# Kernel tuning notes

Hardware: AMD Instinct MI355X
Metric: run time of the kernel (lower is better)

Reference implementation:

```python
import jax, jax.numpy as jnp
from jax import lax
import numpy as np

STRIDES = (2, 2)
PADDING = 'SAME'
EPS = 1e-05


def setup_inputs() -> dict:
    key = jax.random.key(0)
    k1, k2, k3 = jax.random.split(key, 3)
    x = jax.random.normal(k1, (16, 64, 64, 256), dtype=jnp.float32)
    # flax default conv kernel init ~ lecun_normal; plain normal scaled is fine for a math reference
    kernel = jax.random.normal(k2, (4, 4, 256, 128), dtype=jnp.float32) * 0.05
    bias = jax.random.normal(k3, (128,), dtype=jnp.float32) * 0.01
    alpha = jnp.ones((1,), dtype=jnp.float32)
    return {'x': x, 'kernel': kernel, 'bias': bias, 'alpha': alpha}


def reference(x, kernel, bias, alpha):
    # x: [B, H, W, Cin] NHWC; kernel: [kh, kw, Cin, Cout]
    out_features = kernel.shape[-1]

    # main transposed conv: dot-product map  [B, H*2, W*2, Cout]
    dot = lax.conv_transpose(x, kernel, STRIDES, PADDING, transpose_kernel=False)

    # patch squared-sum map: conv_transpose of x**2 with an all-ones kernel
    # of shape kernel_size + (Cin, 1); broadcast over Cout (same math as jnp.repeat)
    ones_k = jnp.ones(kernel.shape[:-1] + (1,), dtype=kernel.dtype)
    patch_sq = lax.conv_transpose(x * x, ones_k, STRIDES, PADDING, transpose_kernel=False)  # [B, H', W', 1]

    # per-filter kernel squared norm, reduced over (kh, kw, Cin) -> [Cout]
    k_sq = jnp.sum(kernel * kernel, axis=(0, 1, 2))

    # ||x_patch - W||^2 = sum(x^2) + sum(W^2) - 2 * <x, W>
    dist_sq = patch_sq + k_sq - 2.0 * dot

    y = (dot * dot) / (dist_sq + EPS)
    y = y + bias  # broadcast over [B, H', W', Cout]

    nf = jnp.float32(out_features)
    scale = (jnp.sqrt(nf) / jnp.log1p(nf)) ** alpha  # alpha shape (1,) broadcasts
    return y * scale
```

## Files before the change

kernel.cpp:

```cpp
#include <hip/hip_runtime.h>
#include <cstdint>
#include <cstddef>

#define CIN   256
#define COUT  128

typedef float  f32x4  __attribute__((ext_vector_type(4)));
typedef __bf16 bf16x8 __attribute__((ext_vector_type(8)));
typedef unsigned int u32x4 __attribute__((ext_vector_type(4)));

#define XPAD_BYTES (16ull*66*66*256*2)
#define WF_OFF     XPAD_BYTES
#define WF_BYTES   (16ull*8*4*128*8*2)
#define SPAD_OFF   (WF_OFF + WF_BYTES)
#define SPAD_BYTES (16ull*66*66*4)
#define KSQ_OFF    (SPAD_OFF + SPAD_BYTES)
#define WS_NEEDED  (KSQ_OFF + 512)

__device__ __forceinline__ unsigned short f2bf(float f) {
  unsigned int u = __float_as_uint(f);
  u += 0x7fffu + ((u >> 16) & 1u);
  return (unsigned short)(u >> 16);
}

__device__ __forceinline__ void async16(const void* lds, const void* g) {
  __builtin_amdgcn_global_load_lds(
      (const __attribute__((address_space(1))) unsigned int*)g,
      (__attribute__((address_space(3))) unsigned int*)lds, 16, 0, 0);
}

__global__ __launch_bounds__(256) void prep_x(
    const float* __restrict__ x, unsigned short* __restrict__ xpad,
    float* __restrict__ spad)
{
  int wave = threadIdx.x >> 6, lane = threadIdx.x & 63;
  int p = blockIdx.x * 4 + wave;
  int b = p / 4356;
  int rem = p - b * 4356;
  int iyp = rem / 66, ixp = rem - iyp * 66;
  bool interior = (iyp >= 1 && iyp <= 64 && ixp >= 1 && ixp <= 64);
  f32x4 v = {0.f, 0.f, 0.f, 0.f};
  if (interior) {
    const float* src = x + (((size_t)b*64 + (iyp-1))*64 + (ixp-1))*CIN + lane*4;
    v = *(const f32x4*)src;
  }
  ushort4 h;
  h.x = f2bf(v.x); h.y = f2bf(v.y); h.z = f2bf(v.z); h.w = f2bf(v.w);
  *(ushort4*)(xpad + (size_t)p*CIN + lane*4) = h;
  float s = v.x*v.x + v.y*v.y + v.z*v.z + v.w*v.w;
  #pragma unroll
  for (int off = 32; off > 0; off >>= 1) s += __shfl_down(s, off);
  if (lane == 0) spad[p] = s;
}

__global__ __launch_bounds__(256) void prep_w2(
    const float* __restrict__ w, unsigned short* __restrict__ wf)
{
  int blk = blockIdx.x;
  int tap = blk >> 3, c8 = blk & 7;
  int t = threadIdx.x;
  #pragma unroll
  for (int rr = 0; rr < 2; ++rr) {
    int row = rr*256 + t;
    int q = row >> 7, co = row & 127;
    union { unsigned short u[8]; uint4 v; } hh;
    #pragma unroll
    for (int e = 0; e < 8; ++e) {
      int ci = c8*32 + q*8 + e;
      hh.u[e] = f2bf(w[((size_t)tap*256 + ci)*COUT + co]);
    }
    *(uint4*)(wf + ((size_t)blk*4 + q)*128*8 + (size_t)co*8) = hh.v;
  }
}

__global__ __launch_bounds__(256) void fb_ksq(const float* __restrict__ w,
                                              float* __restrict__ ksq) {
  __shared__ float red[256];
  int co = blockIdx.x, t = threadIdx.x;
  float s = 0.f;
  for (int j = t; j < 4096; j += 256) { float v = w[(size_t)j*COUT + co]; s += v*v; }
  red[t] = s; __syncthreads();
  for (int off = 128; off > 0; off >>= 1) {
    if (t < off) red[t] += red[t + off];
    __syncthreads();
  }
  if (t == 0) ksq[co] = red[0];
}

__global__ __launch_bounds__(256, 2) void yat_main(
    const unsigned short* __restrict__ xpad,
    const unsigned short* __restrict__ wf,
    const float* __restrict__ spad,
    const float* __restrict__ ksq,
    const float* __restrict__ bias,
    const float* __restrict__ alpha,
    float* __restrict__ out)
{
  __shared__ __align__(16) unsigned short xs[3][4224];
  __shared__ float srow[132];

  int orig = blockIdx.x;
  int bid = (orig & 7) * 256 + (orig >> 3);
  int py = bid & 1, u = (bid >> 1) & 63, b = bid >> 7;
  int t = threadIdx.x, wave = t >> 6, lane = t & 63;
  int px = wave >> 1, coh = wave & 1;
  int l15 = lane & 15, l4 = lane >> 4;

  if (t < 132) {
    int r = t / 66, c = t - r*66;
    srow[t] = spad[((size_t)b*66 + (u + py) + r)*66 + c];
  }

  const size_t xrow = ((size_t)b*66 + (u + py)) * 66 * CIN;

  size_t soff0, soff1, tailoff;
  {
    int s = t;
    int a = s / 264; int r2 = s - a*264;
    int q = r2 / 66; int c = r2 - q*66;
    soff0 = xrow + (size_t)(a*66 + c)*CIN + q*8;
    s = 256 + t;
    a = s / 264; r2 = s - a*264;
    q = r2 / 66; c = r2 - q*66;
    soff1 = xrow + (size_t)(a*66 + c)*CIN + q*8;
    int s2 = 248 + (t & 15);
    int q2 = s2 / 66, c2 = s2 - q2*66;
    tailoff = xrow + (size_t)(66 + c2)*CIN + q2*8;
  }

  unsigned ab_lds = (unsigned)(unsigned long long)(&xs[0][0])
                    + (unsigned)((l4*66 + l15 + px) * 16);
  const unsigned short* wb =
      wf + ((size_t)l4*128 + coh*64 + l15)*8 + (size_t)(py*4 + px)*32768;

  f32x4 acc[4][4];
  #pragma unroll
  for (int i = 0; i < 4; ++i)
    #pragma unroll
    for (int j = 0; j < 4; ++j)
      acc[i][j] = (f32x4){0.f, 0.f, 0.f, 0.f};

  u32x4 B0[2][4], B1[2][4];
  u32x4 Af[2][4];
  u32x4 tvA, tvB;

#define SB  __builtin_amdgcn_sched_barrier(0)
#define BAR __builtin_amdgcn_s_barrier()
#define VMW(N) do { asm volatile("s_waitcnt vmcnt(" #N ")" ::: "memory"); SB; } while (0)
#define LGK(N) do { asm volatile("s_waitcnt lgkmcnt(" #N ")" ::: "memory"); SB; } while (0)

#define GLB(dst, base, off)                                                \
  asm volatile("global_load_dwordx4 %0, %1, off offset:%c2"                \
               : "=v"(dst) : "v"(base), "i"(off))

#define DSR(dst, off)                                                      \
  asm volatile("ds_read_b128 %0, %1 offset:%c2"                            \
               : "=v"(dst) : "v"(ab_lds), "i"(off))

#define STAGE(BUF, K, TV)                                                  \
  {                                                                        \
    async16(&xs[BUF][(size_t)(0*256 + wave*64)*8], xpad + soff0 + (K)*32); \
    async16(&xs[BUF][(size_t)(1*256 + wave*64)*8], xpad + soff1 + (K)*32); \
    SB;                                                                    \
    GLB(TV, (const char*)(xpad + tailoff + (K)*32), 0);                    \
    SB;                                                                    \
  }

#define TAILW(BUF, TV)                                                     \
  { if (t < 16) *((u32x4*)&xs[BUF][(size_t)(512 + t)*8]) = TV; }

#define ISSUEB(BANK, AA, C8)                                               \
  {                                                                        \
    const char* pb0 = (const char*)wb + (AA)*524288 + (C8)*8192;           \
    const char* pb1 = pb0 + 131072;                                        \
    GLB(BANK[0][0], pb0, 0);   GLB(BANK[0][1], pb0, 256);                  \
    GLB(BANK[0][2], pb0, 512); GLB(BANK[0][3], pb0, 768);                  \
    GLB(BANK[1][0], pb1, 0);   GLB(BANK[1][1], pb1, 256);                  \
    GLB(BANK[1][2], pb1, 512); GLB(BANK[1][3], pb1, 768);                  \
    SB;                                                                    \
  }

#define MFMA16(BB, BANK)                                                   \
  {                                                                        \
    _Pragma("unroll")                                                      \
    for (int mt = 0; mt < 4; ++mt)                                         \
      _Pragma("unroll")                                                    \
      for (int nt = 0; nt < 4; ++nt)                                       \
        acc[mt][nt] = __builtin_amdgcn_mfma_f32_16x16x32_bf16(             \
            __builtin_bit_cast(bf16x8, Af[BB][mt]),                        \
            __builtin_bit_cast(bf16x8, BANK[BB][nt]),                      \
            acc[mt][nt], 0, 0, 0);                                         \
  }

#define HALF(N, BUF, A, BANK)                                              \
  {                                                                        \
    VMW(N);                                                                \
    DSR(Af[0][0], (BUF)*8448 + (A)*4224 + 0);                              \
    DSR(Af[0][1], (BUF)*8448 + (A)*4224 + 256);                            \
    DSR(Af[0][2], (BUF)*8448 + (A)*4224 + 512);                            \
    DSR(Af[0][3], (BUF)*8448 + (A)*4224 + 768);                            \
    DSR(Af[1][0], (BUF)*8448 + (A)*4224 + 16);                             \
    DSR(Af[1][1], (BUF)*8448 + (A)*4224 + 272);                            \
    DSR(Af[1][2], (BUF)*8448 + (A)*4224 + 528);                            \
    DSR(Af[1][3], (BUF)*8448 + (A)*4224 + 784);                            \
    LGK(4);                                                                \
    __builtin_amdgcn_s_setprio(1);                                         \
    MFMA16(0, BANK);                                                       \
    LGK(0);                                                                \
    MFMA16(1, BANK);                                                       \
    __builtin_amdgcn_s_setprio(0);                                         \
    SB;                                                                    \
  }

  SB;
  STAGE(0, 0, tvA);
  STAGE(1, 1, tvB);
  ISSUEB(B0, 0, 0);
  ISSUEB(B1, 1, 0);
  VMW(19);
  TAILW(0, tvA); LGK(0); BAR; SB;

  STAGE(2, 2, tvA);
  HALF(11, 0, 0, B0);  ISSUEB(B0, 0, 1);
  HALF(11, 0, 1, B1);  ISSUEB(B1, 1, 1);
  TAILW(1, tvB); LGK(0); BAR; SB;
  STAGE(0, 3, tvB);
  HALF(11, 1, 0, B0);  ISSUEB(B0, 0, 2);
  HALF(11, 1, 1, B1);  ISSUEB(B1, 1, 2);
  TAILW(2, tvA); LGK(0); BAR; SB;
  STAGE(1, 4, tvA);
  HALF(11, 2, 0, B0);  ISSUEB(B0, 0, 3);
  HALF(11, 2, 1, B1);  ISSUEB(B1, 1, 3);
  TAILW(0, tvB); LGK(0); BAR; SB;
  STAGE(2, 5, tvB);
  HALF(11, 0, 0, B0);  ISSUEB(B0, 0, 4);
  HALF(11, 0, 1, B1);  ISSUEB(B1, 1, 4);
  TAILW(1, tvA); LGK(0); BAR; SB;
  STAGE(0, 6, tvA);
  HALF(11, 1, 0, B0);  ISSUEB(B0, 0, 5);
  HALF(11, 1, 1, B1);  ISSUEB(B1, 1, 5);
  TAILW(2, tvB); LGK(0); BAR; SB;
  STAGE(1, 7, tvB);
  HALF(11, 2, 0, B0);  ISSUEB(B0, 0, 6);
  HALF(11, 2, 1, B1);  ISSUEB(B1, 1, 6);
  TAILW(0, tvA); LGK(0); BAR; SB;
  HALF(8, 0, 0, B0);   ISSUEB(B0, 0, 7);
  HALF(8, 0, 1, B1);   ISSUEB(B1, 1, 7);
  TAILW(1, tvB); LGK(0); BAR; SB;
  HALF(8, 1, 0, B0);
  HALF(0, 1, 1, B1);

#undef SB
#undef BAR
#undef VMW
#undef LGK
#undef GLB
#undef DSR
#undef STAGE
#undef TAILW
#undef ISSUEB
#undef MFMA16
#undef HALF

  float scale = powf(sqrtf(128.f) / log1pf(128.f), alpha[0]);
  int oy = 2*u + py;
  float kq[4], bi[4];
  #pragma unroll
  for (int nt = 0; nt < 4; ++nt) {
    int n = coh*64 + nt*16 + l15;
    kq[nt] = ksq[n]; bi[nt] = bias[n];
  }
  size_t orow = ((size_t)b*128 + oy) * 128 * COUT;
  #pragma unroll
  for (int mt = 0; mt < 4; ++mt) {
    #pragma unroll
    for (int r = 0; r < 4; ++r) {
      int v = mt*16 + l4*4 + r;
      float ps = srow[v+px] + srow[v+px+1] + srow[66 + v+px] + srow[66 + v+px+1];
      #pragma unroll
      for (int nt = 0; nt < 4; ++nt) {
        float dot = acc[mt][nt][r];
        float dist = ps + kq[nt] - 2.f*dot + 1e-5f;
        float y = (dot*dot/dist + bi[nt]) * scale;
        int n = coh*64 + nt*16 + l15;
        out[orow + (size_t)(2*v + px)*COUT + n] = y;
      }
    }
  }
}

__global__ __launch_bounds__(256) void fb_main(
    const float* __restrict__ x, const float* __restrict__ w,
    const float* __restrict__ bias, const float* __restrict__ alpha,
    const float* __restrict__ ksq, float* __restrict__ out)
{
  size_t idx = (size_t)blockIdx.x * 256 + threadIdx.x;
  int co = (int)(idx & 127);
  int ox = (int)((idx >> 7) & 127);
  int oy = (int)((idx >> 14) & 127);
  int b  = (int)(idx >> 21);
  int py = oy & 1, px = ox & 1, u = oy >> 1, v = ox >> 1;
  float dot = 0.f, ps = 0.f;
  for (int a = 0; a < 2; ++a) {
    int iy = u + py + a - 1;
    if (iy < 0 || iy > 63) continue;
    for (int b2 = 0; b2 < 2; ++b2) {
      int ix = v + px + b2 - 1;
      if (ix < 0 || ix > 63) continue;
      const float* xp = x + (((size_t)b*64 + iy)*64 + ix)*CIN;
      const float* wp = w + ((size_t)((py + 2*a)*4 + (px + 2*b2))*CIN)*COUT + co;
      for (int ci = 0; ci < CIN; ++ci) {
        float xv = xp[ci];
        dot += xv * wp[(size_t)ci*COUT];
        ps  += xv * xv;
      }
    }
  }
  float dist = ps + ksq[co] - 2.f*dot + 1e-5f;
  float scale = powf(sqrtf(128.f) / log1pf(128.f), alpha[0]);
  out[idx] = (dot*dot/dist + bias[co]) * scale;
}

extern "C" void kernel_launch(void* const* d_in, const int* in_sizes, int n_in,
                              void* d_out, int out_size, void* d_ws, size_t ws_size,
                              hipStream_t stream)
{
  const float* x     = (const float*)d_in[0];
  const float* w     = (const float*)d_in[1];
  const float* bias  = (const float*)d_in[2];
  const float* alpha = (const float*)d_in[3];
  float* out = (float*)d_out;

  if (ws_size < WS_NEEDED) {
    float* ksq = (float*)d_ws;
    fb_ksq<<<128, 256, 0, stream>>>(w, ksq);
    fb_main<<<131072, 256, 0, stream>>>(x, w, bias, alpha, ksq, out);
    return;
  }

  unsigned short* xpad = (unsigned short*)d_ws;
  unsigned short* wfp  = (unsigned short*)((char*)d_ws + WF_OFF);
  float* spad = (float*)((char*)d_ws + SPAD_OFF);
  float* ksq  = (float*)((char*)d_ws + KSQ_OFF);

  fb_ksq<<<128, 256, 0, stream>>>(w, ksq);
  prep_x<<<17424, 256, 0, stream>>>(x, xpad, spad);
  prep_w2<<<128, 256, 0, stream>>>(w, wfp);
  yat_main<<<2048, 256, 0, stream>>>(xpad, wfp, spad, ksq, bias, alpha, out);
}
```

Measured before the change: 113.8 us.

## Compute two output rows per block with 512 threads to share staged input rows

Each block now handles two output rows of the same parity (u2 pairs) with 8 waves. Each wave covers a 32-channel quarter of Cout instead of half and keeps accumulators for both rows. Three input rows are staged in LDS instead of two, so the overlapping middle row is loaded once and reused for both outputs. This halves the grid, and each wave's weight fetch per step shrinks from eight to four dwordx4 loads. The cost is larger LDS use, a more complex tail-staging pattern and a higher thread count per block, which may change occupancy.

Measured after the change: 113.0 us. No clear change (-0.7%).

```diff
diff --git a/kernel.cpp b/kernel.cpp
--- a/kernel.cpp
+++ b/kernel.cpp
@@ -87,7 +87,7 @@
   if (t == 0) ksq[co] = red[0];
 }
 
-__global__ __launch_bounds__(256, 2) void yat_main(
+__global__ __launch_bounds__(512, 2) void yat_main(
     const unsigned short* __restrict__ xpad,
     const unsigned short* __restrict__ wf,
     const float* __restrict__ spad,
@@ -96,51 +96,56 @@
     const float* __restrict__ alpha,
     float* __restrict__ out)
 {
-  __shared__ __align__(16) unsigned short xs[3][4224];
-  __shared__ float srow[132];
+  __shared__ __align__(16) unsigned short xs[3][6336];
+  __shared__ float srow[198];
 
   int orig = blockIdx.x;
-  int bid = (orig & 7) * 256 + (orig >> 3);
-  int py = bid & 1, u = (bid >> 1) & 63, b = bid >> 7;
+  int bid = (orig & 7) * 128 + (orig >> 3);
+  int py = bid & 1, u2 = (bid >> 1) & 31, b = bid >> 6;
   int t = threadIdx.x, wave = t >> 6, lane = t & 63;
-  int px = wave >> 1, coh = wave & 1;
+  int px = wave >> 2, coq = wave & 3;
   int l15 = lane & 15, l4 = lane >> 4;
-
-  if (t < 132) {
+  int base = 2*u2 + py;
+
+  if (t < 198) {
     int r = t / 66, c = t - r*66;
-    srow[t] = spad[((size_t)b*66 + (u + py) + r)*66 + c];
-  }
-
-  const size_t xrow = ((size_t)b*66 + (u + py)) * 66 * CIN;
-
-  size_t soff0, soff1, tailoff;
+    srow[t] = spad[((size_t)b*66 + base + r)*66 + c];
+  }
+
+  const size_t xbase = ((size_t)b*66 + base) * 66 * CIN;
+
+  size_t soff0, soff1, stail;
   {
     int s = t;
-    int a = s / 264; int r2 = s - a*264;
-    int q = r2 / 66; int c = r2 - q*66;
-    soff0 = xrow + (size_t)(a*66 + c)*CIN + q*8;
-    s = 256 + t;
-    a = s / 264; r2 = s - a*264;
-    q = r2 / 66; c = r2 - q*66;
-    soff1 = xrow + (size_t)(a*66 + c)*CIN + q*8;
-    int s2 = 248 + (t & 15);
-    int q2 = s2 / 66, c2 = s2 - q2*66;
-    tailoff = xrow + (size_t)(66 + c2)*CIN + q2*8;
+    int row = s / 264; int r2 = s - row*264;
+    int q = r2 / 66;  int c = r2 - q*66;
+    soff0 = xbase + (size_t)(row*66 + c)*CIN + q*8;
+    s = 512 + (t & 255);
+    row = s / 264; r2 = s - row*264;
+    q = r2 / 66;  c = r2 - q*66;
+    soff1 = xbase + (size_t)(row*66 + c)*CIN + q*8;
+    int ts = t & 31; if (ts > 23) ts = 23;
+    s = 768 + ts;
+    row = s / 264; r2 = s - row*264;
+    q = r2 / 66;  c = r2 - q*66;
+    stail = xbase + (size_t)(row*66 + c)*CIN + q*8;
   }
 
   unsigned ab_lds = (unsigned)(unsigned long long)(&xs[0][0])
                     + (unsigned)((l4*66 + l15 + px) * 16);
   const unsigned short* wb =
-      wf + ((size_t)l4*128 + coh*64 + l15)*8 + (size_t)(py*4 + px)*32768;
-
-  f32x4 acc[4][4];
-  #pragma unroll
-  for (int i = 0; i < 4; ++i)
+      wf + ((size_t)l4*128 + coq*32 + l15)*8 + (size_t)(py*4 + px)*32768;
+
+  f32x4 acc[2][4][2];
+  #pragma unroll
+  for (int j = 0; j < 2; ++j)
     #pragma unroll
-    for (int j = 0; j < 4; ++j)
-      acc[i][j] = (f32x4){0.f, 0.f, 0.f, 0.f};
-
-  u32x4 B0[2][4], B1[2][4];
+    for (int i = 0; i < 4; ++i)
+      #pragma unroll
+      for (int n = 0; n < 2; ++n)
+        acc[j][i][n] = (f32x4){0.f, 0.f, 0.f, 0.f};
+
+  u32x4 B0[2][2], B1[2][2];
   u32x4 Af[2][4];
   u32x4 tvA, tvB;
 
@@ -159,56 +164,56 @@
 
 #define STAGE(BUF, K, TV)                                                  \
   {                                                                        \
-    async16(&xs[BUF][(size_t)(0*256 + wave*64)*8], xpad + soff0 + (K)*32); \
-    async16(&xs[BUF][(size_t)(1*256 + wave*64)*8], xpad + soff1 + (K)*32); \
+    async16(&xs[BUF][(size_t)(wave*64)*8],            xpad + soff0 + (K)*32); \
+    async16(&xs[BUF][(size_t)(512 + (wave&3)*64)*8],  xpad + soff1 + (K)*32); \
     SB;                                                                    \
-    GLB(TV, (const char*)(xpad + tailoff + (K)*32), 0);                    \
+    GLB(TV, (const char*)(xpad + stail + (K)*32), 0);                      \
     SB;                                                                    \
   }
 
 #define TAILW(BUF, TV)                                                     \
-  { if (t < 16) *((u32x4*)&xs[BUF][(size_t)(512 + t)*8]) = TV; }
+  { if (t < 24) *((u32x4*)&xs[BUF][(size_t)(768 + t)*8]) = TV; }
 
 #define ISSUEB(BANK, AA, C8)                                               \
   {                                                                        \
     const char* pb0 = (const char*)wb + (AA)*524288 + (C8)*8192;           \
     const char* pb1 = pb0 + 131072;                                        \
-    GLB(BANK[0][0], pb0, 0);   GLB(BANK[0][1], pb0, 256);                  \
-    GLB(BANK[0][2], pb0, 512); GLB(BANK[0][3], pb0, 768);                  \
-    GLB(BANK[1][0], pb1, 0);   GLB(BANK[1][1], pb1, 256);                  \
-    GLB(BANK[1][2], pb1, 512); GLB(BANK[1][3], pb1, 768);                  \
+    GLB(BANK[0][0], pb0, 0); GLB(BANK[0][1], pb0, 256);                    \
+    GLB(BANK[1][0], pb1, 0); GLB(BANK[1][1], pb1, 256);                    \
     SB;                                                                    \
   }
 
-#define MFMA16(BB, BANK)                                                   \
+#define DSRA(J, A, BUF)                                                    \
+    DSR(Af[0][0], (BUF)*12672 + ((J)+(A))*4224 + 0);                       \
+    DSR(Af[0][1], (BUF)*12672 + ((J)+(A))*4224 + 256);                     \
+    DSR(Af[0][2], (BUF)*12672 + ((J)+(A))*4224 + 512);                     \
+    DSR(Af[0][3], (BUF)*12672 + ((J)+(A))*4224 + 768);                     \
+    DSR(Af[1][0], (BUF)*12672 + ((J)+(A))*4224 + 16);                      \
+    DSR(Af[1][1], (BUF)*12672 + ((J)+(A))*4224 + 272);                     \
+    DSR(Af[1][2], (BUF)*12672 + ((J)+(A))*4224 + 528);                     \
+    DSR(Af[1][3], (BUF)*12672 + ((J)+(A))*4224 + 784);
+
+#define MFMA8(J, BB, BANK)                                                 \
   {                                                                        \
     _Pragma("unroll")                                                      \
     for (int mt = 0; mt < 4; ++mt)                                         \
       _Pragma("unroll")                                                    \
-      for (int nt = 0; nt < 4; ++nt)                                       \
-        acc[mt][nt] = __builtin_amdgcn_mfma_f32_16x16x32_bf16(             \
+      for (int nt = 0; nt < 2; ++nt)                                       \
+        acc[J][mt][nt] = __builtin_amdgcn_mfma_f32_16x16x32_bf16(          \
             __builtin_bit_cast(bf16x8, Af[BB][mt]),                        \
             __builtin_bit_cast(bf16x8, BANK[BB][nt]),                      \
-            acc[mt][nt], 0, 0, 0);                                         \
+            acc[J][mt][nt], 0, 0, 0);                                      \
   }
 
 #define HALF(N, BUF, A, BANK)                                              \
   {                                                                        \
     VMW(N);                                                                \
-    DSR(Af[0][0], (BUF)*8448 + (A)*4224 + 0);                              \
-    DSR(Af[0][1], (BUF)*8448 + (A)*4224 + 256);                            \
-    DSR(Af[0][2], (BUF)*8448 + (A)*4224 + 512);                            \
-    DSR(Af[0][3], (BUF)*8448 + (A)*4224 + 768);                            \
-    DSR(Af[1][0], (BUF)*8448 + (A)*4224 + 16);                             \
-    DSR(Af[1][1], (BUF)*8448 + (A)*4224 + 272);                            \
-    DSR(Af[1][2], (BUF)*8448 + (A)*4224 + 528);                            \
-    DSR(Af[1][3], (BUF)*8448 + (A)*4224 + 784);                            \
-    LGK(4);                                                                \
-    __builtin_amdgcn_s_setprio(1);                                         \
-    MFMA16(0, BANK);                                                       \
-    LGK(0);                                                                \
-    MFMA16(1, BANK);                                                       \
-    __builtin_amdgcn_s_setprio(0);                                         \
+    DSRA(0, A, BUF); LGK(4);                                               \
+    __builtin_amdgcn_s_setprio(1); MFMA8(0, 0, BANK); LGK(0);              \
+    MFMA8(0, 1, BANK); __builtin_amdgcn_s_setprio(0);                      \
+    DSRA(1, A, BUF); LGK(4);                                               \
+    __builtin_amdgcn_s_setprio(1); MFMA8(1, 0, BANK); LGK(0);              \
+    MFMA8(1, 1, BANK); __builtin_amdgcn_s_setprio(0);                      \
     SB;                                                                    \
   }
 
@@ -217,37 +222,37 @@
   STAGE(1, 1, tvB);
   ISSUEB(B0, 0, 0);
   ISSUEB(B1, 1, 0);
-  VMW(19);
+  VMW(11);
   TAILW(0, tvA); LGK(0); BAR; SB;
 
   STAGE(2, 2, tvA);
-  HALF(11, 0, 0, B0);  ISSUEB(B0, 0, 1);
-  HALF(11, 0, 1, B1);  ISSUEB(B1, 1, 1);
+  HALF(7, 0, 0, B0);  ISSUEB(B0, 0, 1);
+  HALF(7, 0, 1, B1);  ISSUEB(B1, 1, 1);
   TAILW(1, tvB); LGK(0); BAR; SB;
   STAGE(0, 3, tvB);
-  HALF(11, 1, 0, B0);  ISSUEB(B0, 0, 2);
-  HALF(11, 1, 1, B1);  ISSUEB(B1, 1, 2);
+  HALF(7, 1, 0, B0);  ISSUEB(B0, 0, 2);
+  HALF(7, 1, 1, B1);  ISSUEB(B1, 1, 2);
   TAILW(2, tvA); LGK(0); BAR; SB;
   STAGE(1, 4, tvA);
-  HALF(11, 2, 0, B0);  ISSUEB(B0, 0, 3);
-  HALF(11, 2, 1, B1);  ISSUEB(B1, 1, 3);
+  HALF(7, 2, 0, B0);  ISSUEB(B0, 0, 3);
+  HALF(7, 2, 1, B1);  ISSUEB(B1, 1, 3);
   TAILW(0, tvB); LGK(0); BAR; SB;
   STAGE(2, 5, tvB);
-  HALF(11, 0, 0, B0);  ISSUEB(B0, 0, 4);
-  HALF(11, 0, 1, B1);  ISSUEB(B1, 1, 4);
+  HALF(7, 0, 0, B0);  ISSUEB(B0, 0, 4);
+  HALF(7, 0, 1, B1);  ISSUEB(B1, 1, 4);
   TAILW(1, tvA); LGK(0); BAR; SB;
   STAGE(0, 6, tvA);
-  HALF(11, 1, 0, B0);  ISSUEB(B0, 0, 5);
-  HALF(11, 1, 1, B1);  ISSUEB(B1, 1, 5);
+  HALF(7, 1, 0, B0);  ISSUEB(B0, 0, 5);
+  HALF(7, 1, 1, B1);  ISSUEB(B1, 1, 5);
   TAILW(2, tvB); LGK(0); BAR; SB;
   STAGE(1, 7, tvB);
-  HALF(11, 2, 0, B0);  ISSUEB(B0, 0, 6);
-  HALF(11, 2, 1, B1);  ISSUEB(B1, 1, 6);
+  HALF(7, 2, 0, B0);  ISSUEB(B0, 0, 6);
+  HALF(7, 2, 1, B1);  ISSUEB(B1, 1, 6);
   TAILW(0, tvA); LGK(0); BAR; SB;
-  HALF(8, 0, 0, B0);   ISSUEB(B0, 0, 7);
-  HALF(8, 0, 1, B1);   ISSUEB(B1, 1, 7);
+  HALF(4, 0, 0, B0);  ISSUEB(B0, 0, 7);
+  HALF(4, 0, 1, B1);  ISSUEB(B1, 1, 7);
   TAILW(1, tvB); LGK(0); BAR; SB;
-  HALF(8, 1, 0, B0);
+  HALF(4, 1, 0, B0);
   HALF(0, 1, 1, B1);
 
 #undef SB
@@ -259,31 +264,38 @@
 #undef STAGE
 #undef TAILW
 #undef ISSUEB
-#undef MFMA16
+#undef DSRA
+#undef MFMA8
 #undef HALF
 
+  __syncthreads();
+
   float scale = powf(sqrtf(128.f) / log1pf(128.f), alpha[0]);
-  int oy = 2*u + py;
-  float kq[4], bi[4];
-  #pragma unroll
-  for (int nt = 0; nt < 4; ++nt) {
-    int n = coh*64 + nt*16 + l15;
+  float kq[2], bi[2];
+  #pragma unroll
+  for (int nt = 0; nt < 2; ++nt) {
+    int n = coq*32 + nt*16 + l15;
     kq[nt] = ksq[n]; bi[nt] = bias[n];
   }
-  size_t orow = ((size_t)b*128 + oy) * 128 * COUT;
-  #pragma unroll
-  for (int mt = 0; mt < 4; ++mt) {
+  #pragma unroll
+  for (int j = 0; j < 2; ++j) {
+    int oy = 4*u2 + 2*j + py;
+    size_t orow = ((size_t)b*128 + oy) * 128 * COUT;
     #pragma unroll
-    for (int r = 0; r < 4; ++r) {
-      int v = mt*16 + l4*4 + r;
-      float ps = srow[v+px] + srow[v+px+1] + srow[66 + v+px] + srow[66 + v+px+1];
+    for (int mt = 0; mt < 4; ++mt) {
       #pragma unroll
-      for (int nt = 0; nt < 4; ++nt) {
-        float dot = acc[mt][nt][r];
-        float dist = ps + kq[nt] - 2.f*dot + 1e-5f;
-        float y = (dot*dot/dist + bi[nt]) * scale;
-        int n = coh*64 + nt*16 + l15;
-        out[orow + (size_t)(2*v + px)*COUT + n] = y;
+      for (int r = 0; r < 4; ++r) {
+        int v = mt*16 + l4*4 + r;
+        float ps = srow[j*66 + v+px] + srow[j*66 + v+px+1]
+                 + srow[(j+1)*66 + v+px] + srow[(j+1)*66 + v+px+1];
+        #pragma unroll
+        for (int nt = 0; nt < 2; ++nt) {
+          float dot = acc[j][mt][nt][r];
+          float dist = ps + kq[nt] - 2.f*dot + 1e-5f;
+          float y = (dot*dot/dist + bi[nt]) * scale;
+          int n = coq*32 + nt*16 + l15;
+          out[orow + (size_t)(2*v + px)*COUT + n] = y;
+        }
       }
     }
   }
@@ -346,5 +358,5 @@
   fb_ksq<<<128, 256, 0, stream>>>(w, ksq);
   prep_x<<<17424, 256, 0, stream>>>(x, xpad, spad);
   prep_w2<<<128, 256, 0, stream>>>(w, wfp);
-  yat_main<<<2048, 256, 0, stream>>>(xpad, wfp, spad, ksq, bias, alpha, out);
-}
+  yat_main<<<1024, 512, 0, stream>>>(xpad, wfp, spad, ksq, bias, alpha, out);
+}
```
